# Kernel tuning notes

Measured on AMD Instinct MI355X. Metric: run time of the kernel, lower is better.

Reference implementation:

```python
import jax, jax.numpy as jnp
import numpy as np

N_USERS = 100000
M_ITEMS = 50000
D = 64
NNZ = 4_000_000
B = 4096
LAYERS = 3


def setup_inputs() -> dict:
    key = jax.random.key(0)
    ks = jax.random.split(key, 7)
    N = N_USERS + M_ITEMS
    return {
        "users": jax.random.randint(ks[0], (B,), 0, N_USERS, dtype=jnp.int64 if jax.config.jax_enable_x64 else jnp.int32),
        "items": jax.random.randint(ks[1], (B,), 0, M_ITEMS, dtype=jnp.int64 if jax.config.jax_enable_x64 else jnp.int32),
        "user_emb": jax.random.normal(ks[2], (N_USERS, D), dtype=jnp.float32) * 0.1,
        "item_emb": jax.random.normal(ks[3], (M_ITEMS, D), dtype=jnp.float32) * 0.1,
        "adj_rows": jax.random.randint(ks[4], (NNZ,), 0, N, dtype=jnp.int32),
        "adj_cols": jax.random.randint(ks[5], (NNZ,), 0, N, dtype=jnp.int32),
        "adj_vals": jax.random.uniform(ks[6], (NNZ,), dtype=jnp.float32),
    }


def reference(users, items, user_emb, item_emb, adj_rows, adj_cols, adj_vals):
    n_users = user_emb.shape[0]
    N = n_users + item_emb.shape[0]

    # computer(): multi-layer sparse propagation, mean over layer outputs
    all_emb = jnp.concatenate([user_emb, item_emb], axis=0)  # [N, D]
    acc = all_emb
    emb = all_emb
    for _ in range(LAYERS):
        # SpMM as gather + segment-sum: (A @ emb)[r] = sum_{e: row(e)=r} val(e) * emb[col(e)]
        messages = adj_vals[:, None] * emb[adj_cols]          # [NNZ, D]
        emb = jax.ops.segment_sum(messages, adj_rows, num_segments=N)
        acc = acc + emb
    light_out = acc / (LAYERS + 1)                            # mean over stacked layers

    all_users = light_out[:n_users]
    all_items = light_out[n_users:]

    # forward(users, items)
    u = all_users[users]                                      # [B, D]
    i = all_items[items]                                      # [B, D]
    gamma = jnp.sum(u * i, axis=1)                            # [B]
    return gamma
```

## Files before the change

kernel.cpp:

```cpp
#include <hip/hip_runtime.h>

#define N_USERS 100000
#define M_ITEMS 50000
#define N_TOTAL (N_USERS + M_ITEMS)
#define D 64
#define NNZ 4000000
#define BATCH 4096

#define RPB 128
#define BSHIFT 7
#define NBUCKETS ((N_TOTAL + RPB - 1) / RPB)
#define BCAP 4352

#define TILE 4096
#define SCAT_BLOCKS ((NNZ + TILE - 1) / TILE)
#define SCAT_THREADS 1024
#define EPT (TILE / SCAT_THREADS)
#define CPB 2

#define LS_THREADS 1024
#define LS_EPT 8

#define INIT_BLOCKS 9375
#define HIST_BLOCKS 512

typedef __attribute__((ext_vector_type(2))) float    f32x2;
typedef __attribute__((ext_vector_type(2))) int      i32x2;

__device__ __forceinline__ unsigned pack_bf16(float a, float b) {
    unsigned ua = __float_as_uint(a);
    unsigned ub = __float_as_uint(b);
    ua = (ua + 0x7FFFu + ((ua >> 16) & 1u)) >> 16;
    ub = (ub + 0x7FFFu + ((ub >> 16) & 1u)) & 0xFFFF0000u;
    return ua | ub;
}

__device__ __forceinline__ f32x2 unpack_bf16x2(unsigned p) {
    union { unsigned u[2]; f32x2 f; } r;
    r.u[0] = p << 16;
    r.u[1] = p & 0xFFFF0000u;
    return r.f;
}

__device__ __forceinline__ int block_scan_incl_1024(int v, int* wsum) {
    int lane = threadIdx.x & 63, wv = threadIdx.x >> 6;
#pragma unroll
    for (int o = 1; o < 64; o <<= 1) {
        int u = __shfl_up(v, o, 64);
        if (lane >= o) v += u;
    }
    if (lane == 63) wsum[wv] = v;
    __syncthreads();
    if (wv == 0) {
        int w = (lane < 16) ? wsum[lane] : 0;
#pragma unroll
        for (int o = 1; o < 16; o <<= 1) {
            int u = __shfl_up(w, o, 64);
            if (lane >= o) w += u;
        }
        if (lane < 16) wsum[lane] = w;
    }
    __syncthreads();
    return v + (wv ? wsum[wv - 1] : 0);
}

__global__ void init_hist_kernel(const float4* __restrict__ ue,
                                 const float4* __restrict__ ie,
                                 uint2* __restrict__ emb,
                                 const int* __restrict__ rows,
                                 int* __restrict__ bucketcnt) {
    __shared__ int h[NBUCKETS];
    if (blockIdx.x < INIT_BLOCKS) {
        size_t i = (size_t)blockIdx.x * 256 + threadIdx.x;
        const size_t nu4 = (size_t)N_USERS * D / 4;
        float4 f = (i < nu4) ? ue[i] : ie[i - nu4];
        emb[i] = make_uint2(pack_bf16(f.x, f.y), pack_bf16(f.z, f.w));
        return;
    }
    int bid = blockIdx.x - INIT_BLOCKS;
    for (int i = threadIdx.x; i < NBUCKETS; i += blockDim.x) h[i] = 0;
    __syncthreads();
    int stride = HIST_BLOCKS * 256;
    for (int e = bid * 256 + threadIdx.x; e < NNZ; e += stride)
        atomicAdd(&h[__builtin_nontemporal_load(rows + e) >> BSHIFT], 1);
    __syncthreads();
    for (int i = threadIdx.x; i < NBUCKETS; i += blockDim.x)
        if (h[i]) atomicAdd(&bucketcnt[i], h[i]);
}

__global__ void bucket_scan_kernel(const int* __restrict__ cnt,
                                   int* __restrict__ bucketoff,
                                   int* __restrict__ cursor) {
    __shared__ int wsum[16];
    int t = threadIdx.x;
    int i0 = t * 2, i1 = t * 2 + 1;
    int a = (i0 < NBUCKETS) ? cnt[i0] : 0;
    int b = (i1 < NBUCKETS) ? cnt[i1] : 0;
    int incl = block_scan_incl_1024(a + b, wsum);
    int excl = incl - a - b;
    if (i0 < NBUCKETS) { bucketoff[i0] = excl;     cursor[i0] = excl; }
    if (i1 < NBUCKETS) { bucketoff[i1] = excl + a; cursor[i1] = excl + a; }
    if (t == 0) bucketoff[NBUCKETS] = NNZ;
}

__global__ __launch_bounds__(SCAT_THREADS)
void bucket_scatter_kernel(const int* __restrict__ rows,
                           const int* __restrict__ cols,
                           const float* __restrict__ vals,
                           int* __restrict__ cursor,
                           int2* __restrict__ bucketed) {
    __shared__ int hist[NBUCKETS];
    __shared__ int loff[NBUCKETS + 1];
    __shared__ int wsum[16];
    __shared__ int2 buf[TILE];
    __shared__ int dst[TILE];
    int t = threadIdx.x;
    size_t start = (size_t)blockIdx.x * TILE;
    int n = (int)(((size_t)NNZ - start < TILE) ? ((size_t)NNZ - start) : TILE);

    for (int i = t; i < NBUCKETS; i += SCAT_THREADS) hist[i] = 0;
    __syncthreads();
    int rowv[EPT];
    int rank[EPT];
#pragma unroll
    for (int k = 0; k < EPT; ++k) {
        int i = t + k * SCAT_THREADS;
        if (i < n) {
            int r = __builtin_nontemporal_load(rows + start + i);
            rowv[k] = r;
            rank[k] = atomicAdd(&hist[r >> BSHIFT], 1);
        }
    }
    __syncthreads();
    {
        int base = t * CPB;
        int s = 0;
#pragma unroll
        for (int j = 0; j < CPB; ++j) {
            int idx = base + j;
            if (idx < NBUCKETS) s += hist[idx];
        }
        int excl = block_scan_incl_1024(s, wsum) - s;
#pragma unroll
        for (int j = 0; j < CPB; ++j) {
            int idx = base + j;
            if (idx < NBUCKETS) { loff[idx] = excl; excl += hist[idx]; }
        }
        if (t == 0) loff[NBUCKETS] = n;
    }
    __syncthreads();
    for (int i = t; i < NBUCKETS; i += SCAT_THREADS) {
        int c = loff[i + 1] - loff[i];
        hist[i] = c ? atomicAdd(&cursor[i], c) : 0;
    }
    __syncthreads();
#pragma unroll
    for (int k = 0; k < EPT; ++k) {
        int i = t + k * SCAT_THREADS;
        if (i < n) {
            int r = rowv[k];
            int bkt = r >> BSHIFT;
            int slot = loff[bkt] + rank[k];
            int cv = __builtin_nontemporal_load(cols + start + i);
            float vv = __builtin_nontemporal_load(vals + start + i);
            buf[slot] = make_int2(((r & (RPB - 1)) << 18) | cv, __float_as_int(vv));
            dst[slot] = hist[bkt] + rank[k];
        }
    }
    __syncthreads();
    for (int i = t; i < n; i += SCAT_THREADS)
        bucketed[dst[i]] = buf[i];
}

__global__ __launch_bounds__(LS_THREADS)
void local_sort_kernel(const int* __restrict__ bucketoff,
                       const int2* __restrict__ bucketed,
                       int* __restrict__ row_start,
                       int2* __restrict__ edges) {
    __shared__ int hist[RPB];
    __shared__ int sc[RPB];
    __shared__ int2 buf[BCAP];
    int b = blockIdx.x;
    int t = threadIdx.x;
    int s = bucketoff[b], e = bucketoff[b + 1], n = e - s;

    if (t < RPB) hist[t] = 0;
    __syncthreads();
    int rl[LS_EPT], rank[LS_EPT];
    int2 pay[LS_EPT];
#pragma unroll
    for (int k = 0; k < LS_EPT; ++k) {
        int i = t + k * LS_THREADS;
        if (i < n) {
            i32x2 ev = __builtin_nontemporal_load((const i32x2*)(bucketed + s + i));
            rl[k] = (int)((unsigned)ev.x >> 18);
            pay[k] = make_int2((ev.x & 0x3FFFF) << 7, ev.y);
            rank[k] = atomicAdd(&hist[rl[k]], 1);
        }
    }
    __syncthreads();
    if (t < RPB) {
        int lane = t & 63;
        int v = hist[t];
#pragma unroll
        for (int o = 1; o < 64; o <<= 1) {
            int u = __shfl_up(v, o, 64);
            if (lane >= o) v += u;
        }
        sc[t] = v;
    }
    __syncthreads();
    if (t >= 64 && t < RPB) sc[t] += sc[63];
    __syncthreads();
    if (t < RPB) {
        int excl = (t == 0) ? 0 : sc[t - 1];
        int gr = b * RPB + t;
        if (gr < N_TOTAL) row_start[gr] = s + excl;
    }
    if (b == 0 && t == 0) row_start[N_TOTAL] = NNZ;
    __syncthreads();
#pragma unroll
    for (int k = 0; k < LS_EPT; ++k) {
        int i = t + k * LS_THREADS;
        if (i < n) {
            int excl = (rl[k] == 0) ? 0 : sc[rl[k] - 1];
            int p = excl + rank[k];
            if (p < BCAP) buf[p] = pay[k];
            else          edges[s + p] = pay[k];
        }
    }
    __syncthreads();
    int m = (n < BCAP) ? n : BCAP;
    for (int i = t; i < m; i += LS_THREADS) edges[s + i] = buf[i];
}


#define EDGE_SLOT(ei, ji)                                                    \
    {                                                                        \
        int   c_  = (ji < n) ? ei.x : 0;                                     \
        float mv_ = (ji < n) ? __int_as_float(ei.y) : 0.0f;                  \
        uint4 p_  = *(const uint4*)(ebase + c_);                             \
        f32x2 vv_ = {mv_, mv_};                                              \
        a01 = __builtin_elementwise_fma(unpack_bf16x2(p_.x), vv_, a01);      \
        a23 = __builtin_elementwise_fma(unpack_bf16x2(p_.y), vv_, a23);      \
        a45 = __builtin_elementwise_fma(unpack_bf16x2(p_.z), vv_, a45);      \
        a67 = __builtin_elementwise_fma(unpack_bf16x2(p_.w), vv_, a67);      \
    }

#define SPMM_BODY(row_s, row_e)                                              \
    int n = (row_e) - (row_s);                                               \
    const int2* ep = edges + (row_s) + oct;                                  \
    f32x2 a01 = {0.f, 0.f}, a23 = {0.f, 0.f};                                \
    f32x2 a45 = {0.f, 0.f}, a67 = {0.f, 0.f};                                \
    int tmax = (n + 7) >> 3;                                                 \
    int t = 0;                                                               \
    for (; t + 4 <= tmax; t += 4) {                                          \
        int2 e0 = ep[0], e1 = ep[8], e2 = ep[16], e3 = ep[24];               \
        ep += 32;                                                            \
        int j0 = (t << 3) + oct;                                             \
        EDGE_SLOT(e0, j0);                                                   \
        EDGE_SLOT(e1, (j0 + 8));                                             \
        EDGE_SLOT(e2, (j0 + 16));                                            \
        EDGE_SLOT(e3, (j0 + 24));                                            \
    }                                                                        \
    if (t + 2 <= tmax) {                                                     \
        int2 e0 = ep[0], e1 = ep[8];                                         \
        ep += 16;                                                            \
        int j0 = (t << 3) + oct;                                             \
        EDGE_SLOT(e0, j0);                                                   \
        EDGE_SLOT(e1, (j0 + 8));                                             \
        t += 2;                                                              \
    }                                                                        \
    if (t < tmax) {                                                          \
        int2 e0 = ep[0];                                                     \
        int j0 = (t << 3) + oct;                                             \
        EDGE_SLOT(e0, j0);                                                   \
    }                                                                        \
    _Pragma("unroll")                                                        \
    for (int o = 8; o <= 32; o <<= 1) {                                      \
        a01.x += __shfl_xor(a01.x, o, 64); a01.y += __shfl_xor(a01.y, o, 64);\
        a23.x += __shfl_xor(a23.x, o, 64); a23.y += __shfl_xor(a23.y, o, 64);\
        a45.x += __shfl_xor(a45.x, o, 64); a45.y += __shfl_xor(a45.y, o, 64);\
        a67.x += __shfl_xor(a67.x, o, 64); a67.y += __shfl_xor(a67.y, o, 64);\
    }

__global__ void spmm_csr_kernel(const int* __restrict__ row_start,
                                const int2* __restrict__ edges,
                                const char* __restrict__ emb_in,
                                uint4* __restrict__ emb_out) {
    int wave = (blockIdx.x * blockDim.x + threadIdx.x) >> 6;
    int lane = threadIdx.x & 63;
    if (wave >= N_TOTAL) return;
    int oct = lane >> 3;
    int ui  = lane & 7;
    const char* ebase = emb_in + (ui << 4);
    int s = row_start[wave];
    int e = row_start[wave + 1];
    SPMM_BODY(s, e);
    if (oct == 0)
        emb_out[(size_t)wave * 8 + ui] =
            make_uint4(pack_bf16(a01.x, a01.y), pack_bf16(a23.x, a23.y),
                       pack_bf16(a45.x, a45.y), pack_bf16(a67.x, a67.y));
}

__global__ void finalize_kernel(const int* __restrict__ users,
                                const int* __restrict__ items,
                                const float* __restrict__ ue,
                                const float* __restrict__ ie,
                                const int* __restrict__ row_start,
                                const int2* __restrict__ edges,
                                const char* __restrict__ embB,
                                const char* __restrict__ embA,
                                float* __restrict__ out) {
    int wave = (blockIdx.x * blockDim.x + threadIdx.x) >> 6;
    int lane = threadIdx.x & 63;
    if (wave >= BATCH) return;
    int oct = lane >> 3;
    int ui  = lane & 7;
    const char* ebase = embA + (ui << 4);

    int ru = users[wave];
    int ri = N_USERS + items[wave];

    f32x2 u01, u23, u45, u67, i01, i23, i45, i67;
    {
        SPMM_BODY(row_start[ru], row_start[ru + 1]);
        u01 = a01; u23 = a23; u45 = a45; u67 = a67;
    }
    {
        SPMM_BODY(row_start[ri], row_start[ri + 1]);
        i01 = a01; i23 = a23; i45 = a45; i67 = a67;
    }

    {
        const float4* up = (const float4*)(ue + (size_t)ru * D + 8 * ui);
        float4 f0 = up[0], f1 = up[1];
        u01 += (f32x2){f0.x, f0.y}; u23 += (f32x2){f0.z, f0.w};
        u45 += (f32x2){f1.x, f1.y}; u67 += (f32x2){f1.z, f1.w};
        uint4 pb = *(const uint4*)(embB + (size_t)ru * 128 + (ui << 4));
        uint4 pa = *(const uint4*)(embA + (size_t)ru * 128 + (ui << 4));
        u01 += unpack_bf16x2(pb.x) + unpack_bf16x2(pa.x);
        u23 += unpack_bf16x2(pb.y) + unpack_bf16x2(pa.y);
        u45 += unpack_bf16x2(pb.z) + unpack_bf16x2(pa.z);
        u67 += unpack_bf16x2(pb.w) + unpack_bf16x2(pa.w);
    }
    {
        const float4* ip = (const float4*)(ie + (size_t)items[wave] * D + 8 * ui);
        float4 f0 = ip[0], f1 = ip[1];
        i01 += (f32x2){f0.x, f0.y}; i23 += (f32x2){f0.z, f0.w};
        i45 += (f32x2){f1.x, f1.y}; i67 += (f32x2){f1.z, f1.w};
        uint4 pb = *(const uint4*)(embB + (size_t)ri * 128 + (ui << 4));
        uint4 pa = *(const uint4*)(embA + (size_t)ri * 128 + (ui << 4));
        i01 += unpack_bf16x2(pb.x) + unpack_bf16x2(pa.x);
        i23 += unpack_bf16x2(pb.y) + unpack_bf16x2(pa.y);
        i45 += unpack_bf16x2(pb.z) + unpack_bf16x2(pa.z);
        i67 += unpack_bf16x2(pb.w) + unpack_bf16x2(pa.w);
    }

    f32x2 d = u01 * i01;
    d = __builtin_elementwise_fma(u23, i23, d);
    d = __builtin_elementwise_fma(u45, i45, d);
    d = __builtin_elementwise_fma(u67, i67, d);
    float p = d.x + d.y;
#pragma unroll
    for (int o = 1; o <= 4; o <<= 1) p += __shfl_xor(p, o, 64);
    if (lane == 0) out[wave] = p * (1.0f / 16.0f);
}


extern "C" void kernel_launch(void* const* d_in, const int* in_sizes, int n_in,
                              void* d_out, int out_size, void* d_ws, size_t ws_size,
                              hipStream_t stream) {
    const int*   users = (const int*)d_in[0];
    const int*   items = (const int*)d_in[1];
    const float* ue    = (const float*)d_in[2];
    const float* ie    = (const float*)d_in[3];
    const int*   rows  = (const int*)d_in[4];
    const int*   cols  = (const int*)d_in[5];
    const float* vals  = (const float*)d_in[6];
    float*       out   = (float*)d_out;

    char* ws = (char*)d_ws;
    size_t off = 0;
    auto alloc = [&](size_t bytes) {
        void* p = ws + off;
        off += (bytes + 255) & ~(size_t)255;
        return p;
    };
    const size_t NBH = (size_t)N_TOTAL * D * sizeof(unsigned short);
    char*  embA      = (char*)alloc(NBH);
    char*  embB      = (char*)alloc(NBH);
    int*   row_start = (int*)alloc(((size_t)N_TOTAL + 1) * sizeof(int));
    int*   bucketcnt = (int*)alloc((size_t)NBUCKETS * sizeof(int));
    int*   bucketoff = (int*)alloc(((size_t)NBUCKETS + 1) * sizeof(int));
    int*   cursor    = (int*)alloc((size_t)NBUCKETS * sizeof(int));
    int2*  edges     = (int2*)alloc((size_t)NNZ * sizeof(int2) + 256);
    int2*  bucketed  = (int2*)alloc((size_t)NNZ * sizeof(int2));

    hipMemsetAsync(bucketcnt, 0, (size_t)NBUCKETS * sizeof(int), stream);
    init_hist_kernel<<<INIT_BLOCKS + HIST_BLOCKS, 256, 0, stream>>>(
        (const float4*)ue, (const float4*)ie, (uint2*)embA, rows, bucketcnt);
    bucket_scan_kernel<<<1, 1024, 0, stream>>>(bucketcnt, bucketoff, cursor);
    bucket_scatter_kernel<<<SCAT_BLOCKS, SCAT_THREADS, 0, stream>>>(
        rows, cols, vals, cursor, bucketed);
    local_sort_kernel<<<NBUCKETS, LS_THREADS, 0, stream>>>(
        bucketoff, bucketed, row_start, edges);

    spmm_csr_kernel<<<(N_TOTAL * 64 + 255) / 256, 256, 0, stream>>>(
        row_start, edges, embA, (uint4*)embB);

    spmm_csr_kernel<<<(N_TOTAL * 64 + 255) / 256, 256, 0, stream>>>(
        row_start, edges, embB, (uint4*)embA);

    finalize_kernel<<<(BATCH * 64 + 255) / 256, 256, 0, stream>>>(
        users, items, ue, ie, row_start, edges, embB, embA, out);
}
```

Before: 342.4 us.

## Replace two-pass bucket sort CSR build with per-row counts and direct atomic scatter

```diff
diff --git a/kernel.cpp b/kernel.cpp
--- a/kernel.cpp
+++ b/kernel.cpp
@@ -10,19 +10,13 @@
 #define RPB 128
 #define BSHIFT 7
 #define NBUCKETS ((N_TOTAL + RPB - 1) / RPB)
-#define BCAP 4352
-
-#define TILE 4096
-#define SCAT_BLOCKS ((NNZ + TILE - 1) / TILE)
-#define SCAT_THREADS 1024
-#define EPT (TILE / SCAT_THREADS)
-#define CPB 2
-
-#define LS_THREADS 1024
-#define LS_EPT 8
 
 #define INIT_BLOCKS 9375
 #define HIST_BLOCKS 512
+
+#define DS_THREADS 256
+#define DS_EPT 8
+#define DS_BLOCKS ((NNZ + DS_THREADS * DS_EPT - 1) / (DS_THREADS * DS_EPT))
 
 typedef __attribute__((ext_vector_type(2))) float    f32x2;
 typedef __attribute__((ext_vector_type(2))) int      i32x2;
@@ -68,7 +62,8 @@
                                  const float4* __restrict__ ie,
                                  uint2* __restrict__ emb,
                                  const int* __restrict__ rows,
-                                 int* __restrict__ bucketcnt) {
+                                 int* __restrict__ bucketcnt,
+                                 int* __restrict__ rowcnt) {
     __shared__ int h[NBUCKETS];
     if (blockIdx.x < INIT_BLOCKS) {
         size_t i = (size_t)blockIdx.x * 256 + threadIdx.x;
@@ -81,16 +76,18 @@
     for (int i = threadIdx.x; i < NBUCKETS; i += blockDim.x) h[i] = 0;
     __syncthreads();
     int stride = HIST_BLOCKS * 256;
-    for (int e = bid * 256 + threadIdx.x; e < NNZ; e += stride)
-        atomicAdd(&h[__builtin_nontemporal_load(rows + e) >> BSHIFT], 1);
+    for (int e = bid * 256 + threadIdx.x; e < NNZ; e += stride) {
+        int r = __builtin_nontemporal_load(rows + e);
+        atomicAdd(&h[r >> BSHIFT], 1);
+        atomicAdd(&rowcnt[r], 1);
+    }
     __syncthreads();
     for (int i = threadIdx.x; i < NBUCKETS; i += blockDim.x)
         if (h[i]) atomicAdd(&bucketcnt[i], h[i]);
 }
 
 __global__ void bucket_scan_kernel(const int* __restrict__ cnt,
-                                   int* __restrict__ bucketoff,
-                                   int* __restrict__ cursor) {
+                                   int* __restrict__ bucketoff) {
     __shared__ int wsum[16];
     int t = threadIdx.x;
     int i0 = t * 2, i1 = t * 2 + 1;
@@ -98,140 +95,62 @@
     int b = (i1 < NBUCKETS) ? cnt[i1] : 0;
     int incl = block_scan_incl_1024(a + b, wsum);
     int excl = incl - a - b;
-    if (i0 < NBUCKETS) { bucketoff[i0] = excl;     cursor[i0] = excl; }
-    if (i1 < NBUCKETS) { bucketoff[i1] = excl + a; cursor[i1] = excl + a; }
-    if (t == 0) bucketoff[NBUCKETS] = NNZ;
-}
-
-__global__ __launch_bounds__(SCAT_THREADS)
-void bucket_scatter_kernel(const int* __restrict__ rows,
+    if (i0 < NBUCKETS) bucketoff[i0] = excl;
+    if (i1 < NBUCKETS) bucketoff[i1] = excl + a;
+}
+
+__global__ void row_scan_kernel(const int* __restrict__ rowcnt,
+                                const int* __restrict__ bucketoff,
+                                int* __restrict__ row_start,
+                                int* __restrict__ row_cursor) {
+    __shared__ int w0;
+    int b = blockIdx.x;
+    int t = threadIdx.x;
+    int gr = b * RPB + t;
+    int v = (gr < N_TOTAL) ? rowcnt[gr] : 0;
+    int lane = t & 63;
+    int incl = v;
+#pragma unroll
+    for (int o = 1; o < 64; o <<= 1) {
+        int u = __shfl_up(incl, o, 64);
+        if (lane >= o) incl += u;
+    }
+    if (t == 63) w0 = incl;
+    __syncthreads();
+    if (t >= 64) incl += w0;
+    int rs = bucketoff[b] + incl - v;
+    if (gr < N_TOTAL) { row_start[gr] = rs; row_cursor[gr] = rs; }
+    if (b == 0 && t == 0) row_start[N_TOTAL] = NNZ;
+}
+
+__global__ __launch_bounds__(DS_THREADS)
+void direct_scatter_kernel(const int* __restrict__ rows,
                            const int* __restrict__ cols,
                            const float* __restrict__ vals,
-                           int* __restrict__ cursor,
-                           int2* __restrict__ bucketed) {
-    __shared__ int hist[NBUCKETS];
-    __shared__ int loff[NBUCKETS + 1];
-    __shared__ int wsum[16];
-    __shared__ int2 buf[TILE];
-    __shared__ int dst[TILE];
-    int t = threadIdx.x;
-    size_t start = (size_t)blockIdx.x * TILE;
-    int n = (int)(((size_t)NNZ - start < TILE) ? ((size_t)NNZ - start) : TILE);
-
-    for (int i = t; i < NBUCKETS; i += SCAT_THREADS) hist[i] = 0;
-    __syncthreads();
-    int rowv[EPT];
-    int rank[EPT];
-#pragma unroll
-    for (int k = 0; k < EPT; ++k) {
-        int i = t + k * SCAT_THREADS;
-        if (i < n) {
-            int r = __builtin_nontemporal_load(rows + start + i);
-            rowv[k] = r;
-            rank[k] = atomicAdd(&hist[r >> BSHIFT], 1);
+                           int* __restrict__ row_cursor,
+                           int2* __restrict__ edges) {
+    int base = blockIdx.x * (DS_THREADS * DS_EPT) + threadIdx.x;
+    int r[DS_EPT], c[DS_EPT], p[DS_EPT];
+    float v[DS_EPT];
+#pragma unroll
+    for (int k = 0; k < DS_EPT; ++k) {
+        int e = base + k * DS_THREADS;
+        if (e < NNZ) {
+            r[k] = __builtin_nontemporal_load(rows + e);
+            c[k] = __builtin_nontemporal_load(cols + e);
+            v[k] = __builtin_nontemporal_load(vals + e);
         }
     }
-    __syncthreads();
-    {
-        int base = t * CPB;
-        int s = 0;
-#pragma unroll
-        for (int j = 0; j < CPB; ++j) {
-            int idx = base + j;
-            if (idx < NBUCKETS) s += hist[idx];
-        }
-        int excl = block_scan_incl_1024(s, wsum) - s;
-#pragma unroll
-        for (int j = 0; j < CPB; ++j) {
-            int idx = base + j;
-            if (idx < NBUCKETS) { loff[idx] = excl; excl += hist[idx]; }
-        }
-        if (t == 0) loff[NBUCKETS] = n;
-    }
-    __syncthreads();
-    for (int i = t; i < NBUCKETS; i += SCAT_THREADS) {
-        int c = loff[i + 1] - loff[i];
-        hist[i] = c ? atomicAdd(&cursor[i], c) : 0;
-    }
-    __syncthreads();
-#pragma unroll
-    for (int k = 0; k < EPT; ++k) {
-        int i = t + k * SCAT_THREADS;
-        if (i < n) {
-            int r = rowv[k];
-            int bkt = r >> BSHIFT;
-            int slot = loff[bkt] + rank[k];
-            int cv = __builtin_nontemporal_load(cols + start + i);
-            float vv = __builtin_nontemporal_load(vals + start + i);
-            buf[slot] = make_int2(((r & (RPB - 1)) << 18) | cv, __float_as_int(vv));
-            dst[slot] = hist[bkt] + rank[k];
-        }
-    }
-    __syncthreads();
-    for (int i = t; i < n; i += SCAT_THREADS)
-        bucketed[dst[i]] = buf[i];
-}
-
-__global__ __launch_bounds__(LS_THREADS)
-void local_sort_kernel(const int* __restrict__ bucketoff,
-                       const int2* __restrict__ bucketed,
-                       int* __restrict__ row_start,
-                       int2* __restrict__ edges) {
-    __shared__ int hist[RPB];
-    __shared__ int sc[RPB];
-    __shared__ int2 buf[BCAP];
-    int b = blockIdx.x;
-    int t = threadIdx.x;
-    int s = bucketoff[b], e = bucketoff[b + 1], n = e - s;
-
-    if (t < RPB) hist[t] = 0;
-    __syncthreads();
-    int rl[LS_EPT], rank[LS_EPT];
-    int2 pay[LS_EPT];
-#pragma unroll
-    for (int k = 0; k < LS_EPT; ++k) {
-        int i = t + k * LS_THREADS;
-        if (i < n) {
-            i32x2 ev = __builtin_nontemporal_load((const i32x2*)(bucketed + s + i));
-            rl[k] = (int)((unsigned)ev.x >> 18);
-            pay[k] = make_int2((ev.x & 0x3FFFF) << 7, ev.y);
-            rank[k] = atomicAdd(&hist[rl[k]], 1);
-        }
-    }
-    __syncthreads();
-    if (t < RPB) {
-        int lane = t & 63;
-        int v = hist[t];
-#pragma unroll
-        for (int o = 1; o < 64; o <<= 1) {
-            int u = __shfl_up(v, o, 64);
-            if (lane >= o) v += u;
-        }
-        sc[t] = v;
-    }
-    __syncthreads();
-    if (t >= 64 && t < RPB) sc[t] += sc[63];
-    __syncthreads();
-    if (t < RPB) {
-        int excl = (t == 0) ? 0 : sc[t - 1];
-        int gr = b * RPB + t;
-        if (gr < N_TOTAL) row_start[gr] = s + excl;
-    }
-    if (b == 0 && t == 0) row_start[N_TOTAL] = NNZ;
-    __syncthreads();
-#pragma unroll
-    for (int k = 0; k < LS_EPT; ++k) {
-        int i = t + k * LS_THREADS;
-        if (i < n) {
-            int excl = (rl[k] == 0) ? 0 : sc[rl[k] - 1];
-            int p = excl + rank[k];
-            if (p < BCAP) buf[p] = pay[k];
-            else          edges[s + p] = pay[k];
-        }
-    }
-    __syncthreads();
-    int m = (n < BCAP) ? n : BCAP;
-    for (int i = t; i < m; i += LS_THREADS) edges[s + i] = buf[i];
+#pragma unroll
+    for (int k = 0; k < DS_EPT; ++k) {
+        int e = base + k * DS_THREADS;
+        if (e < NNZ) p[k] = atomicAdd(&row_cursor[r[k]], 1);
+    }
+#pragma unroll
+    for (int k = 0; k < DS_EPT; ++k) {
+        int e = base + k * DS_THREADS;
+        if (e < NNZ) edges[p[k]] = make_int2(c[k] << 7, __float_as_int(v[k]));
+    }
 }
 
 
@@ -388,23 +307,26 @@
         return p;
     };
     const size_t NBH = (size_t)N_TOTAL * D * sizeof(unsigned short);
-    char*  embA      = (char*)alloc(NBH);
-    char*  embB      = (char*)alloc(NBH);
-    int*   row_start = (int*)alloc(((size_t)N_TOTAL + 1) * sizeof(int));
-    int*   bucketcnt = (int*)alloc((size_t)NBUCKETS * sizeof(int));
-    int*   bucketoff = (int*)alloc(((size_t)NBUCKETS + 1) * sizeof(int));
-    int*   cursor    = (int*)alloc((size_t)NBUCKETS * sizeof(int));
-    int2*  edges     = (int2*)alloc((size_t)NNZ * sizeof(int2) + 256);
-    int2*  bucketed  = (int2*)alloc((size_t)NNZ * sizeof(int2));
-
+    char*  embA       = (char*)alloc(NBH);
+    char*  embB       = (char*)alloc(NBH);
+    int*   row_start  = (int*)alloc(((size_t)N_TOTAL + 1) * sizeof(int));
+    int*   rowcnt     = (int*)alloc((size_t)N_TOTAL * sizeof(int));
+    int*   row_cursor = (int*)alloc((size_t)N_TOTAL * sizeof(int));
+    int*   bucketcnt  = (int*)alloc((size_t)NBUCKETS * sizeof(int));
+    int*   bucketoff  = (int*)alloc((size_t)NBUCKETS * sizeof(int));
+    int2*  edges      = (int2*)alloc((size_t)NNZ * sizeof(int2) + 256);
+
+    hipMemsetAsync(rowcnt, 0, (size_t)N_TOTAL * sizeof(int), stream);
     hipMemsetAsync(bucketcnt, 0, (size_t)NBUCKETS * sizeof(int), stream);
+
     init_hist_kernel<<<INIT_BLOCKS + HIST_BLOCKS, 256, 0, stream>>>(
-        (const float4*)ue, (const float4*)ie, (uint2*)embA, rows, bucketcnt);
-    bucket_scan_kernel<<<1, 1024, 0, stream>>>(bucketcnt, bucketoff, cursor);
-    bucket_scatter_kernel<<<SCAT_BLOCKS, SCAT_THREADS, 0, stream>>>(
-        rows, cols, vals, cursor, bucketed);
-    local_sort_kernel<<<NBUCKETS, LS_THREADS, 0, stream>>>(
-        bucketoff, bucketed, row_start, edges);
+        (const float4*)ue, (const float4*)ie, (uint2*)embA, rows,
+        bucketcnt, rowcnt);
+    bucket_scan_kernel<<<1, 1024, 0, stream>>>(bucketcnt, bucketoff);
+    row_scan_kernel<<<NBUCKETS, RPB, 0, stream>>>(
+        rowcnt, bucketoff, row_start, row_cursor);
+    direct_scatter_kernel<<<DS_BLOCKS, DS_THREADS, 0, stream>>>(
+        rows, cols, vals, row_cursor, edges);
 
     spmm_csr_kernel<<<(N_TOTAL * 64 + 255) / 256, 256, 0, stream>>>(
         row_start, edges, embA, (uint4*)embB);
```

Result: slower. 660.9 us (+93.0%).
